# Optimization experiments

Hardware: AMD Instinct MI355X
Metric: run time of the kernel (lower is better)

## Reference

```python
import jax, jax.numpy as jnp
import numpy as np

CUTN = 32
CUT_SIZE = 224
CUT_POW = 1.0


def _adaptive_avg_pool2d(crop, out_size):
    """Faithful torch F.adaptive_avg_pool2d for a square NCHW crop (static size).
    Uses a summed-area table so each output pixel averages the exact torch bin
    [floor(i*S/out), ceil((i+1)*S/out))."""
    S = crop.shape[2]
    idx = np.arange(out_size)
    s = (idx * S) // out_size                       # bin starts
    e = ((idx + 1) * S + out_size - 1) // out_size  # bin ends (ceil)
    # summed-area table, padded so P[..., i, j] = sum over crop[..., :i, :j]
    P = jnp.pad(jnp.cumsum(jnp.cumsum(crop, axis=2), axis=3),
                ((0, 0), (0, 0), (1, 0), (1, 0)))
    A = (P[:, :, e][:, :, :, e] - P[:, :, s][:, :, :, e]
         - P[:, :, e][:, :, :, s] + P[:, :, s][:, :, :, s])
    cnt = (e - s).astype(np.float32)
    return A / jnp.asarray(np.outer(cnt, cnt), crop.dtype)


def setup_inputs() -> dict:
    key = jax.random.key(0)
    B, C, H, W = 8, 3, 512, 512
    x = jax.random.normal(key, (B, C, H, W), dtype=jnp.float32)
    # Replicate torch's host-side RNG with a fixed numpy generator so sizes and
    # offsets are deterministic constants (in-range by construction).
    rng = np.random.default_rng(0)
    max_size = min(H, W)
    min_size = min(H, W, CUT_SIZE)
    sizes, oy, ox = [], [], []
    for _ in range(CUTN):
        sz = int(rng.random() ** CUT_POW * (max_size - min_size) + min_size)
        sizes.append(sz)
        oy.append(int(rng.integers(0, H - sz + 1)))
        ox.append(int(rng.integers(0, W - sz + 1)))
    return {
        "x": x,
        "sizes": jnp.asarray(sizes, jnp.int32),
        "offsets_y": jnp.asarray(oy, jnp.int32),
        "offsets_x": jnp.asarray(ox, jnp.int32),
        "cut_size": CUT_SIZE,
    }


def reference(x, sizes, offsets_y, offsets_x, cut_size):
    B, C, _, _ = x.shape
    sizes_np = np.asarray(sizes)
    oy_np = np.asarray(offsets_y)
    ox_np = np.asarray(offsets_x)
    cutouts = []
    for i in range(sizes_np.shape[0]):  # loop over fixed cutn (structural)
        sz = int(sizes_np[i])
        crop = jax.lax.dynamic_slice(
            x, (0, 0, int(oy_np[i]), int(ox_np[i])), (B, C, sz, sz))
        cutouts.append(_adaptive_avg_pool2d(crop, cut_size))
    return jnp.concatenate(cutouts, axis=0)  # [cutn*B, C, cut_size, cut_size]
```

## Files before the change

### kernel.cpp

```cpp
#include <hip/hip_runtime.h>


typedef float f32x4 __attribute__((ext_vector_type(4)));

constexpr int OUTSZ = 224;
constexpr int BB    = 8;
constexpr int CC    = 3;
constexpr int HH    = 512;
constexpr int WW    = 512;
constexpr int CUTN  = 32;

constexpr int TP     = 8;
constexpr int NBAND  = OUTSZ / TP;
constexpr int LDSF   = TP * WW + 8;
constexpr int NPLANE = BB * CC;
constexpr int WPP    = CUTN * NBAND;
constexpr int NBLOCKS = NPLANE * WPP;
constexpr int NXCD   = 8;
constexpr int CHUNK  = NBLOCKS / NXCD;

template <int WIN>
__device__ __forceinline__ void pool_cols(const float* __restrict__ tile,
                                          float* __restrict__ outp,
                                          int base, const float* __restrict__ w)
{
#pragma unroll
    for (int k = 0; k < TP; ++k) {
        const float* tr = tile + k * WW + base;
        float s = tr[0] * w[0];
        s = fmaf(tr[1], w[1], s);
        s = fmaf(tr[2], w[2], s);
        if (WIN == 4) s = fmaf(tr[3], w[3], s);
        outp[(size_t)k * OUTSZ] = s;
    }
}

__global__ __launch_bounds__(256, 8) void make_cutouts_kernel(
    const float* __restrict__ x,
    const int*   __restrict__ sizes,
    const int*   __restrict__ offy,
    const int*   __restrict__ offx,
    float*       __restrict__ out)
{
    __shared__ float tile[LDSF];

    int gid = blockIdx.x;
    int w   = (gid % NXCD) * CHUNK + gid / NXCD;

    int plane = w / WPP;
    int rest  = w - plane * WPP;
    int i     = rest / NBAND;
    int tb    = rest - i * NBAND;
    int b     = plane / CC;
    int c     = plane - b * CC;

    int S  = sizes[i];
    int y0 = offy[i];
    int x0 = offx[i];
    int p0 = tb * TP;
    int tid = threadIdx.x;

    const float* plane_p = x + (size_t)(plane * HH + y0) * WW;

    if (tid < 8) tile[TP * WW + tid] = 0.0f;

    int wv   = __builtin_amdgcn_readfirstlane(tid >> 6);
    int lane = tid & 63;
    int vo   = ((wv & 1) << 6) + lane;
    f32x4* tile4 = (f32x4*)tile;
#pragma unroll
    for (int j = 0; j < 4; ++j) {
        int k  = (wv >> 1) + 2 * j;
        int p  = p0 + k;
        int rs = (p * S) / OUTSZ;
        int wp = ((p + 1) * S + OUTSZ - 1) / OUTSZ - rs;
        const f32x4* rp = (const f32x4*)(plane_p + (size_t)rs * WW);
        f32x4 a = rp[vo];
        f32x4 v1, v2, v3;
        bool b1 = wp > 1, b2 = wp > 2, b3 = wp > 3;
        if (b1) v1 = rp[vo + 128];
        if (b2) v2 = rp[vo + 256];
        if (b3) v3 = rp[vo + 384];
        if (b1) a += v1;
        if (b2) a += v2;
        if (b3) a += v3;
        float iv = (wp == 1) ? 1.0f : (wp == 2) ? 0.5f
                 : (wp == 3) ? (1.0f / 3.0f) : 0.25f;
        a *= iv;
        tile4[k * 128 + vo] = a;
    }
    __syncthreads();

    if (tid < OUTSZ) {
        int q  = tid;
        int sq = (q * S) / OUTSZ;
        int wq = ((q + 1) * S + OUTSZ - 1) / OUTSZ - sq;
        float invq = (wq == 1) ? 1.0f : (wq == 2) ? 0.5f
                   : (wq == 3) ? (1.0f / 3.0f) : 0.25f;
        float wt[4];
        wt[0] = invq;
        wt[1] = (wq > 1) ? invq : 0.0f;
        wt[2] = (wq > 2) ? invq : 0.0f;
        wt[3] = (wq > 3) ? invq : 0.0f;
        float* outp = out
            + ((size_t)((i * BB + b) * CC + c) * OUTSZ + p0) * OUTSZ + q;
        if (S <= 2 * OUTSZ)
            pool_cols<3>(tile, outp, x0 + sq, wt);
        else
            pool_cols<4>(tile, outp, x0 + sq, wt);
    }
}

extern "C" void kernel_launch(void* const* d_in, const int* in_sizes, int n_in,
                              void* d_out, int out_size, void* d_ws, size_t ws_size,
                              hipStream_t stream) {
    const float* x     = (const float*)d_in[0];
    const int*   sizes = (const int*)d_in[1];
    const int*   offy  = (const int*)d_in[2];
    const int*   offx  = (const int*)d_in[3];
    float* out = (float*)d_out;

    make_cutouts_kernel<<<NBLOCKS, 256, 0, stream>>>(x, sizes, offy, offx, out);
}
```

Before: 194.0 us.

## Make each block loop over all bands with double-buffered LDS pipeline

Switches from one block per 8-row band to one block per (plane, cutout) that walks all 28 bands. Global loads for band k+2 are issued into registers while band k+1 is written to LDS and band k is pooled, using a double-buffered tile. This hides global load latency within a block and amortizes setup such as the column weights. In exchange there are only 768 blocks, with more LDS and registers per block and lower occupancy (launch bounds 3), so less parallelism is available to hide latency.

```diff
diff --git a/kernel.cpp b/kernel.cpp
--- a/kernel.cpp
+++ b/kernel.cpp
@@ -12,21 +12,60 @@
 
 constexpr int TP     = 8;
 constexpr int NBAND  = OUTSZ / TP;
-constexpr int LDSF   = TP * WW + 8;
+constexpr int TILEF  = TP * WW + 8;
 constexpr int NPLANE = BB * CC;
-constexpr int WPP    = CUTN * NBAND;
-constexpr int NBLOCKS = NPLANE * WPP;
+constexpr int NBLOCKS = NPLANE * CUTN;
 constexpr int NXCD   = 8;
 constexpr int CHUNK  = NBLOCKS / NXCD;
 
+__device__ __forceinline__ void stage_issue(const float* __restrict__ plane_p,
+                                            int S, int p0, int wv, int vo,
+                                            f32x4 (&v)[4][4])
+{
+#pragma unroll
+    for (int j = 0; j < 4; ++j) {
+        int k  = (wv >> 1) + 2 * j;
+        int p  = p0 + k;
+        int rs = (p * S) / OUTSZ;
+        int wp = ((p + 1) * S + OUTSZ - 1) / OUTSZ - rs;
+        const f32x4* rp = (const f32x4*)(plane_p + (size_t)rs * WW);
+        v[j][0] = rp[vo];
+        if (wp > 1) v[j][1] = rp[vo + 128];
+        if (wp > 2) v[j][2] = rp[vo + 256];
+        if (wp > 3) v[j][3] = rp[vo + 384];
+    }
+}
+
+__device__ __forceinline__ void stage_write(float* __restrict__ buf,
+                                            int S, int p0, int wv, int vo,
+                                            f32x4 (&v)[4][4])
+{
+    f32x4* t4 = (f32x4*)buf;
+#pragma unroll
+    for (int j = 0; j < 4; ++j) {
+        int k  = (wv >> 1) + 2 * j;
+        int p  = p0 + k;
+        int rs = (p * S) / OUTSZ;
+        int wp = ((p + 1) * S + OUTSZ - 1) / OUTSZ - rs;
+        f32x4 a = v[j][0];
+        if (wp > 1) a += v[j][1];
+        if (wp > 2) a += v[j][2];
+        if (wp > 3) a += v[j][3];
+        float iv = (wp == 1) ? 1.0f : (wp == 2) ? 0.5f
+                 : (wp == 3) ? (1.0f / 3.0f) : 0.25f;
+        a *= iv;
+        t4[k * 128 + vo] = a;
+    }
+}
+
 template <int WIN>
-__device__ __forceinline__ void pool_cols(const float* __restrict__ tile,
+__device__ __forceinline__ void pool_band(const float* __restrict__ buf,
                                           float* __restrict__ outp,
                                           int base, const float* __restrict__ w)
 {
 #pragma unroll
     for (int k = 0; k < TP; ++k) {
-        const float* tr = tile + k * WW + base;
+        const float* tr = buf + k * WW + base;
         float s = tr[0] * w[0];
         s = fmaf(tr[1], w[1], s);
         s = fmaf(tr[2], w[2], s);
@@ -35,80 +74,85 @@
     }
 }
 
-__global__ __launch_bounds__(256, 8) void make_cutouts_kernel(
+__device__ __forceinline__ void band_barrier()
+{
+    asm volatile("s_waitcnt lgkmcnt(0)" ::: "memory");
+    __builtin_amdgcn_s_barrier();
+}
+
+template <int WIN>
+__device__ __forceinline__ void run_bands(const float* __restrict__ plane_p,
+                                          float (*tile)[TILEF],
+                                          float* __restrict__ outp,
+                                          int S, int wv, int vo, int tid,
+                                          int base, const float* __restrict__ wt,
+                                          f32x4 (&v)[4][4])
+{
+    for (int k = 0; k < NBAND; ++k) {
+        if (k + 1 < NBAND)
+            stage_write(tile[(k + 1) & 1], S, (k + 1) * TP, wv, vo, v);
+        if (k + 2 < NBAND)
+            stage_issue(plane_p, S, (k + 2) * TP, wv, vo, v);
+        if (tid < OUTSZ)
+            pool_band<WIN>(tile[k & 1], outp + (size_t)k * TP * OUTSZ, base, wt);
+        band_barrier();
+    }
+}
+
+__global__ __launch_bounds__(256, 3) void make_cutouts_kernel(
     const float* __restrict__ x,
     const int*   __restrict__ sizes,
     const int*   __restrict__ offy,
     const int*   __restrict__ offx,
     float*       __restrict__ out)
 {
-    __shared__ float tile[LDSF];
+    __shared__ float tile[2][TILEF];
 
     int gid = blockIdx.x;
     int w   = (gid % NXCD) * CHUNK + gid / NXCD;
-
-    int plane = w / WPP;
-    int rest  = w - plane * WPP;
-    int i     = rest / NBAND;
-    int tb    = rest - i * NBAND;
+    int plane = w / CUTN;
+    int i     = w - plane * CUTN;
     int b     = plane / CC;
     int c     = plane - b * CC;
 
     int S  = sizes[i];
     int y0 = offy[i];
     int x0 = offx[i];
-    int p0 = tb * TP;
     int tid = threadIdx.x;
 
     const float* plane_p = x + (size_t)(plane * HH + y0) * WW;
 
-    if (tid < 8) tile[TP * WW + tid] = 0.0f;
+    if (tid < 8) {
+        tile[0][TP * WW + tid] = 0.0f;
+        tile[1][TP * WW + tid] = 0.0f;
+    }
 
     int wv   = __builtin_amdgcn_readfirstlane(tid >> 6);
     int lane = tid & 63;
     int vo   = ((wv & 1) << 6) + lane;
-    f32x4* tile4 = (f32x4*)tile;
-#pragma unroll
-    for (int j = 0; j < 4; ++j) {
-        int k  = (wv >> 1) + 2 * j;
-        int p  = p0 + k;
-        int rs = (p * S) / OUTSZ;
-        int wp = ((p + 1) * S + OUTSZ - 1) / OUTSZ - rs;
-        const f32x4* rp = (const f32x4*)(plane_p + (size_t)rs * WW);
-        f32x4 a = rp[vo];
-        f32x4 v1, v2, v3;
-        bool b1 = wp > 1, b2 = wp > 2, b3 = wp > 3;
-        if (b1) v1 = rp[vo + 128];
-        if (b2) v2 = rp[vo + 256];
-        if (b3) v3 = rp[vo + 384];
-        if (b1) a += v1;
-        if (b2) a += v2;
-        if (b3) a += v3;
-        float iv = (wp == 1) ? 1.0f : (wp == 2) ? 0.5f
-                 : (wp == 3) ? (1.0f / 3.0f) : 0.25f;
-        a *= iv;
-        tile4[k * 128 + vo] = a;
-    }
-    __syncthreads();
 
-    if (tid < OUTSZ) {
-        int q  = tid;
-        int sq = (q * S) / OUTSZ;
-        int wq = ((q + 1) * S + OUTSZ - 1) / OUTSZ - sq;
-        float invq = (wq == 1) ? 1.0f : (wq == 2) ? 0.5f
-                   : (wq == 3) ? (1.0f / 3.0f) : 0.25f;
-        float wt[4];
-        wt[0] = invq;
-        wt[1] = (wq > 1) ? invq : 0.0f;
-        wt[2] = (wq > 2) ? invq : 0.0f;
-        wt[3] = (wq > 3) ? invq : 0.0f;
-        float* outp = out
-            + ((size_t)((i * BB + b) * CC + c) * OUTSZ + p0) * OUTSZ + q;
-        if (S <= 2 * OUTSZ)
-            pool_cols<3>(tile, outp, x0 + sq, wt);
-        else
-            pool_cols<4>(tile, outp, x0 + sq, wt);
-    }
+    int sq = (tid * S) / OUTSZ;
+    int wq = ((tid + 1) * S + OUTSZ - 1) / OUTSZ - sq;
+    float invq = (wq == 1) ? 1.0f : (wq == 2) ? 0.5f
+               : (wq == 3) ? (1.0f / 3.0f) : 0.25f;
+    float wt[4];
+    wt[0] = invq;
+    wt[1] = (wq > 1) ? invq : 0.0f;
+    wt[2] = (wq > 2) ? invq : 0.0f;
+    wt[3] = (wq > 3) ? invq : 0.0f;
+    int base = x0 + sq;
+    float* outp = out + ((size_t)((i * BB + b) * CC + c) * OUTSZ) * OUTSZ + tid;
+
+    f32x4 v[4][4];
+    stage_issue(plane_p, S, 0, wv, vo, v);
+    stage_write(tile[0], S, 0, wv, vo, v);
+    stage_issue(plane_p, S, TP, wv, vo, v);
+    band_barrier();
+
+    if (S <= 2 * OUTSZ)
+        run_bands<3>(plane_p, tile, outp, S, wv, vo, tid, base, wt, v);
+    else
+        run_bands<4>(plane_p, tile, outp, S, wv, vo, tid, base, wt, v);
 }
 
 extern "C" void kernel_launch(void* const* d_in, const int* in_sizes, int n_in,
```

Result: slower. 220.3 us (+13.5%).

## Make each wavefront process its own output rows with double-buffered LDS slices

Applied to the files above, without the earlier changes.

Each wavefront now independently processes 4 output rows, using its own double-buffered LDS row slice instead of a shared 8-row tile. This removes the block-wide __syncthreads. It also prefetches the next row's global loads into registers while the current row is pooled along x. Block size per band grows to 16 rows, so there are half as many blocks. The per-wave scheme depends on wave-synchronous LDS visibility without a barrier, and it uses more registers.

```diff
diff --git a/kernel.cpp b/kernel.cpp
--- a/kernel.cpp
+++ b/kernel.cpp
@@ -10,28 +10,88 @@
 constexpr int WW    = 512;
 constexpr int CUTN  = 32;
 
-constexpr int TP     = 8;
-constexpr int NBAND  = OUTSZ / TP;
-constexpr int LDSF   = TP * WW + 8;
+constexpr int RPB    = 16;
+constexpr int RPW    = 4;
+constexpr int NCH    = OUTSZ / RPB;
+constexpr int SLICEF = WW + 8;
 constexpr int NPLANE = BB * CC;
-constexpr int WPP    = CUTN * NBAND;
-constexpr int NBLOCKS = NPLANE * WPP;
+constexpr int NBLOCKS = NPLANE * CUTN * NCH;
 constexpr int NXCD   = 8;
-constexpr int CHUNK  = NBLOCKS / NXCD;
+constexpr int CHUNKSZ = NBLOCKS / NXCD;
+
+__device__ __forceinline__ void load_row(const float* __restrict__ plane_p,
+                                         int S, int p, int lane, f32x4 (&v)[8])
+{
+    int rs = (p * S) / OUTSZ;
+    int wp = ((p + 1) * S + OUTSZ - 1) / OUTSZ - rs;
+    const f32x4* rp = (const f32x4*)(plane_p + (size_t)rs * WW);
+    int c0 = lane;
+    int c1 = lane + 64;
+    v[0] = rp[c0];        v[1] = rp[c1];
+    if (wp > 1) { v[2] = rp[c0 + 128]; v[3] = rp[c1 + 128]; }
+    if (wp > 2) { v[4] = rp[c0 + 256]; v[5] = rp[c1 + 256]; }
+    if (wp > 3) { v[6] = rp[c0 + 384]; v[7] = rp[c1 + 384]; }
+}
+
+__device__ __forceinline__ void reduce_write(float* __restrict__ buf,
+                                             int S, int p, int lane,
+                                             f32x4 (&v)[8])
+{
+    int rs = (p * S) / OUTSZ;
+    int wp = ((p + 1) * S + OUTSZ - 1) / OUTSZ - rs;
+    f32x4 a0 = v[0], a1 = v[1];
+    if (wp > 1) { a0 += v[2]; a1 += v[3]; }
+    if (wp > 2) { a0 += v[4]; a1 += v[5]; }
+    if (wp > 3) { a0 += v[6]; a1 += v[7]; }
+    float iv = (wp == 1) ? 1.0f : (wp == 2) ? 0.5f
+             : (wp == 3) ? (1.0f / 3.0f) : 0.25f;
+    a0 *= iv; a1 *= iv;
+    f32x4* t4 = (f32x4*)buf;
+    t4[lane] = a0;
+    t4[lane + 64] = a1;
+}
 
 template <int WIN>
-__device__ __forceinline__ void pool_cols(const float* __restrict__ tile,
-                                          float* __restrict__ outp,
-                                          int base, const float* __restrict__ w)
+__device__ __forceinline__ void pool_row(const float* __restrict__ buf,
+                                         float* __restrict__ outrow,
+                                         int x0, int lane,
+                                         const int* __restrict__ sqv,
+                                         const int* __restrict__ wqv,
+                                         const float* __restrict__ invqv)
 {
 #pragma unroll
-    for (int k = 0; k < TP; ++k) {
-        const float* tr = tile + k * WW + base;
-        float s = tr[0] * w[0];
-        s = fmaf(tr[1], w[1], s);
-        s = fmaf(tr[2], w[2], s);
-        if (WIN == 4) s = fmaf(tr[3], w[3], s);
-        outp[(size_t)k * OUTSZ] = s;
+    for (int m = 0; m < 4; ++m) {
+        if (m == 3 && lane >= 32) break;
+        const float* tr = buf + x0 + sqv[m];
+        float z = 0.0f;
+        float s = tr[0];
+        s += (wqv[m] > 1) ? tr[1] : z;
+        s += (wqv[m] > 2) ? tr[2] : z;
+        if (WIN == 4) s += (wqv[m] > 3) ? tr[3] : z;
+        outrow[lane + 64 * m] = s * invqv[m];
+    }
+}
+
+template <int WIN>
+__device__ __forceinline__ void run_rows(const float* __restrict__ plane_p,
+                                         float* __restrict__ s0,
+                                         float* __restrict__ s1,
+                                         float* __restrict__ outbase,
+                                         int S, int x0, int p0, int lane,
+                                         const int* __restrict__ sqv,
+                                         const int* __restrict__ wqv,
+                                         const float* __restrict__ invqv)
+{
+    f32x4 v[8];
+    load_row(plane_p, S, p0, lane, v);
+#pragma unroll
+    for (int r = 0; r < RPW; ++r) {
+        float* buf = (r & 1) ? s1 : s0;
+        reduce_write(buf, S, p0 + r, lane, v);
+        if (r + 1 < RPW)
+            load_row(plane_p, S, p0 + r + 1, lane, v);
+        pool_row<WIN>(buf, outbase + (size_t)(p0 + r) * OUTSZ,
+                      x0, lane, sqv, wqv, invqv);
     }
 }
 
@@ -42,73 +102,50 @@
     const int*   __restrict__ offx,
     float*       __restrict__ out)
 {
-    __shared__ float tile[LDSF];
+    __shared__ float lds[4][2][SLICEF];
 
     int gid = blockIdx.x;
-    int w   = (gid % NXCD) * CHUNK + gid / NXCD;
-
-    int plane = w / WPP;
-    int rest  = w - plane * WPP;
-    int i     = rest / NBAND;
-    int tb    = rest - i * NBAND;
+    int w   = (gid % NXCD) * CHUNKSZ + gid / NXCD;
+    int plane = w / (CUTN * NCH);
+    int rest  = w - plane * (CUTN * NCH);
+    int i     = rest / NCH;
+    int ch    = rest - i * NCH;
     int b     = plane / CC;
     int c     = plane - b * CC;
 
     int S  = sizes[i];
     int y0 = offy[i];
     int x0 = offx[i];
-    int p0 = tb * TP;
-    int tid = threadIdx.x;
+    int tid  = threadIdx.x;
+    int wv   = __builtin_amdgcn_readfirstlane(tid >> 6);
+    int lane = tid & 63;
+    int p0   = ch * RPB + wv * RPW;
 
     const float* plane_p = x + (size_t)(plane * HH + y0) * WW;
+    float* s0 = &lds[wv][0][0];
+    float* s1 = &lds[wv][1][0];
 
-    if (tid < 8) tile[TP * WW + tid] = 0.0f;
+    int   sqv[4];
+    int   wqv[4];
+    float invqv[4];
+#pragma unroll
+    for (int m = 0; m < 4; ++m) {
+        int q = lane + 64 * m;
+        int qq = (q < OUTSZ) ? q : 0;
+        int sq = (qq * S) / OUTSZ;
+        int wq = ((qq + 1) * S + OUTSZ - 1) / OUTSZ - sq;
+        sqv[m] = sq;
+        wqv[m] = wq;
+        invqv[m] = (wq == 1) ? 1.0f : (wq == 2) ? 0.5f
+                 : (wq == 3) ? (1.0f / 3.0f) : 0.25f;
+    }
 
-    int wv   = __builtin_amdgcn_readfirstlane(tid >> 6);
-    int lane = tid & 63;
-    int vo   = ((wv & 1) << 6) + lane;
-    f32x4* tile4 = (f32x4*)tile;
-#pragma unroll
-    for (int j = 0; j < 4; ++j) {
-        int k  = (wv >> 1) + 2 * j;
-        int p  = p0 + k;
-        int rs = (p * S) / OUTSZ;
-        int wp = ((p + 1) * S + OUTSZ - 1) / OUTSZ - rs;
-        const f32x4* rp = (const f32x4*)(plane_p + (size_t)rs * WW);
-        f32x4 a = rp[vo];
-        f32x4 v1, v2, v3;
-        bool b1 = wp > 1, b2 = wp > 2, b3 = wp > 3;
-        if (b1) v1 = rp[vo + 128];
-        if (b2) v2 = rp[vo + 256];
-        if (b3) v3 = rp[vo + 384];
-        if (b1) a += v1;
-        if (b2) a += v2;
-        if (b3) a += v3;
-        float iv = (wp == 1) ? 1.0f : (wp == 2) ? 0.5f
-                 : (wp == 3) ? (1.0f / 3.0f) : 0.25f;
-        a *= iv;
-        tile4[k * 128 + vo] = a;
-    }
-    __syncthreads();
+    float* outbase = out + (size_t)((i * BB + b) * CC + c) * OUTSZ * OUTSZ;
 
-    if (tid < OUTSZ) {
-        int q  = tid;
-        int sq = (q * S) / OUTSZ;
-        int wq = ((q + 1) * S + OUTSZ - 1) / OUTSZ - sq;
-        float invq = (wq == 1) ? 1.0f : (wq == 2) ? 0.5f
-                   : (wq == 3) ? (1.0f / 3.0f) : 0.25f;
-        float wt[4];
-        wt[0] = invq;
-        wt[1] = (wq > 1) ? invq : 0.0f;
-        wt[2] = (wq > 2) ? invq : 0.0f;
-        wt[3] = (wq > 3) ? invq : 0.0f;
-        float* outp = out
-            + ((size_t)((i * BB + b) * CC + c) * OUTSZ + p0) * OUTSZ + q;
-        if (S <= 2 * OUTSZ)
-            pool_cols<3>(tile, outp, x0 + sq, wt);
-        else
-            pool_cols<4>(tile, outp, x0 + sq, wt);
-    }
+    if (S <= 2 * OUTSZ)
+        run_rows<3>(plane_p, s0, s1, outbase, S, x0, p0, lane, sqv, wqv, invqv);
+    else
+        run_rows<4>(plane_p, s0, s1, outbase, S, x0, p0, lane, sqv, wqv, invqv);
 }
 
 extern "C" void kernel_launch(void* const* d_in, const int* in_sizes, int n_in,
```

Result: slower. 247.5 us (+27.5%).

## Split row band into two halves and overlap second-half loads with first-half pooling

Applied to the files above, without the earlier changes.

The 8-row band is processed in two halves of 4 rows. The global loads for the second half are issued into registers before the first half is written to LDS and column-pooled, so memory latency is hidden behind the first half's pooling and stores. A custom barrier waits only on LDS counters rather than doing a full syncthreads. This raises register pressure (two sets of 8 f32x4 load buffers) under the 8-blocks-per-SM launch bound, and adds a second barrier per block.

```diff
diff --git a/kernel.cpp b/kernel.cpp
--- a/kernel.cpp
+++ b/kernel.cpp
@@ -19,20 +19,87 @@
 constexpr int NXCD   = 8;
 constexpr int CHUNK  = NBLOCKS / NXCD;
 
-template <int WIN>
-__device__ __forceinline__ void pool_cols(const float* __restrict__ tile,
-                                          float* __restrict__ outp,
-                                          int base, const float* __restrict__ w)
+__device__ __forceinline__ void half_issue(const float* __restrict__ plane_p,
+                                           int S, int p0h, int wv, int vo,
+                                           f32x4 (&v)[2][4])
 {
 #pragma unroll
-    for (int k = 0; k < TP; ++k) {
-        const float* tr = tile + k * WW + base;
+    for (int j = 0; j < 2; ++j) {
+        int k  = (wv >> 1) + 2 * j;
+        int p  = p0h + k;
+        int rs = (p * S) / OUTSZ;
+        int wp = ((p + 1) * S + OUTSZ - 1) / OUTSZ - rs;
+        const f32x4* rp = (const f32x4*)(plane_p + (size_t)rs * WW);
+        v[j][0] = rp[vo];
+        if (wp > 1) v[j][1] = rp[vo + 128];
+        if (wp > 2) v[j][2] = rp[vo + 256];
+        if (wp > 3) v[j][3] = rp[vo + 384];
+    }
+}
+
+__device__ __forceinline__ void half_write(float* __restrict__ tile,
+                                           int S, int p0h, int rowoff,
+                                           int wv, int vo, f32x4 (&v)[2][4])
+{
+    f32x4* t4 = (f32x4*)tile;
+#pragma unroll
+    for (int j = 0; j < 2; ++j) {
+        int k  = (wv >> 1) + 2 * j;
+        int p  = p0h + k;
+        int rs = (p * S) / OUTSZ;
+        int wp = ((p + 1) * S + OUTSZ - 1) / OUTSZ - rs;
+        f32x4 a = v[j][0];
+        if (wp > 1) a += v[j][1];
+        if (wp > 2) a += v[j][2];
+        if (wp > 3) a += v[j][3];
+        float iv = (wp == 1) ? 1.0f : (wp == 2) ? 0.5f
+                 : (wp == 3) ? (1.0f / 3.0f) : 0.25f;
+        a *= iv;
+        t4[(rowoff + k) * 128 + vo] = a;
+    }
+}
+
+template <int WIN>
+__device__ __forceinline__ void pool_half(const float* __restrict__ tile,
+                                          float* __restrict__ outp,
+                                          int rowoff, int base,
+                                          const float* __restrict__ w)
+{
+#pragma unroll
+    for (int k = 0; k < 4; ++k) {
+        const float* tr = tile + (rowoff + k) * WW + base;
         float s = tr[0] * w[0];
         s = fmaf(tr[1], w[1], s);
         s = fmaf(tr[2], w[2], s);
         if (WIN == 4) s = fmaf(tr[3], w[3], s);
         outp[(size_t)k * OUTSZ] = s;
     }
+}
+
+__device__ __forceinline__ void lgkm_barrier()
+{
+    asm volatile("s_waitcnt lgkmcnt(0)" ::: "memory");
+    __builtin_amdgcn_s_barrier();
+}
+
+template <int WIN>
+__device__ __forceinline__ void run_block(const float* __restrict__ plane_p,
+                                          float* __restrict__ tile,
+                                          float* __restrict__ outp,
+                                          int S, int p0, int wv, int vo,
+                                          int tid, int base,
+                                          const float* __restrict__ wt,
+                                          f32x4 (&vA)[2][4], f32x4 (&vB)[2][4])
+{
+    half_write(tile, S, p0, 0, wv, vo, vA);
+    half_issue(plane_p, S, p0 + 4, wv, vo, vB);
+    lgkm_barrier();
+    if (tid < OUTSZ)
+        pool_half<WIN>(tile, outp, 0, base, wt);
+    half_write(tile, S, p0 + 4, 4, wv, vo, vB);
+    lgkm_barrier();
+    if (tid < OUTSZ)
+        pool_half<WIN>(tile, outp + (size_t)4 * OUTSZ, 4, base, wt);
 }
 
 __global__ __launch_bounds__(256, 8) void make_cutouts_kernel(
@@ -46,7 +113,6 @@
 
     int gid = blockIdx.x;
     int w   = (gid % NXCD) * CHUNK + gid / NXCD;
-
     int plane = w / WPP;
     int rest  = w - plane * WPP;
     int i     = rest / NBAND;
@@ -62,53 +128,32 @@
 
     const float* plane_p = x + (size_t)(plane * HH + y0) * WW;
 
-    if (tid < 8) tile[TP * WW + tid] = 0.0f;
-
     int wv   = __builtin_amdgcn_readfirstlane(tid >> 6);
     int lane = tid & 63;
     int vo   = ((wv & 1) << 6) + lane;
-    f32x4* tile4 = (f32x4*)tile;
-#pragma unroll
-    for (int j = 0; j < 4; ++j) {
-        int k  = (wv >> 1) + 2 * j;
-        int p  = p0 + k;
-        int rs = (p * S) / OUTSZ;
-        int wp = ((p + 1) * S + OUTSZ - 1) / OUTSZ - rs;
-        const f32x4* rp = (const f32x4*)(plane_p + (size_t)rs * WW);
-        f32x4 a = rp[vo];
-        f32x4 v1, v2, v3;
-        bool b1 = wp > 1, b2 = wp > 2, b3 = wp > 3;
-        if (b1) v1 = rp[vo + 128];
-        if (b2) v2 = rp[vo + 256];
-        if (b3) v3 = rp[vo + 384];
-        if (b1) a += v1;
-        if (b2) a += v2;
-        if (b3) a += v3;
-        float iv = (wp == 1) ? 1.0f : (wp == 2) ? 0.5f
-                 : (wp == 3) ? (1.0f / 3.0f) : 0.25f;
-        a *= iv;
-        tile4[k * 128 + vo] = a;
-    }
-    __syncthreads();
 
-    if (tid < OUTSZ) {
-        int q  = tid;
-        int sq = (q * S) / OUTSZ;
-        int wq = ((q + 1) * S + OUTSZ - 1) / OUTSZ - sq;
-        float invq = (wq == 1) ? 1.0f : (wq == 2) ? 0.5f
-                   : (wq == 3) ? (1.0f / 3.0f) : 0.25f;
-        float wt[4];
-        wt[0] = invq;
-        wt[1] = (wq > 1) ? invq : 0.0f;
-        wt[2] = (wq > 2) ? invq : 0.0f;
-        wt[3] = (wq > 3) ? invq : 0.0f;
-        float* outp = out
-            + ((size_t)((i * BB + b) * CC + c) * OUTSZ + p0) * OUTSZ + q;
-        if (S <= 2 * OUTSZ)
-            pool_cols<3>(tile, outp, x0 + sq, wt);
-        else
-            pool_cols<4>(tile, outp, x0 + sq, wt);
-    }
+    f32x4 vA[2][4], vB[2][4];
+    half_issue(plane_p, S, p0, wv, vo, vA);
+
+    if (tid < 8) tile[TP * WW + tid] = 0.0f;
+
+    int sq = (tid * S) / OUTSZ;
+    int wq = ((tid + 1) * S + OUTSZ - 1) / OUTSZ - sq;
+    float invq = (wq == 1) ? 1.0f : (wq == 2) ? 0.5f
+               : (wq == 3) ? (1.0f / 3.0f) : 0.25f;
+    float wt[4];
+    wt[0] = invq;
+    wt[1] = (wq > 1) ? invq : 0.0f;
+    wt[2] = (wq > 2) ? invq : 0.0f;
+    wt[3] = (wq > 3) ? invq : 0.0f;
+    int base = x0 + sq;
+    float* outp = out
+        + ((size_t)((i * BB + b) * CC + c) * OUTSZ + p0) * OUTSZ + tid;
+
+    if (S <= 2 * OUTSZ)
+        run_block<3>(plane_p, tile, outp, S, p0, wv, vo, tid, base, wt, vA, vB);
+    else
+        run_block<4>(plane_p, tile, outp, S, p0, wv, vo, tid, base, wt, vA, vB);
 }
 
 extern "C" void kernel_launch(void* const* d_in, const int* in_sizes, int n_in,
```

After: 204.0 us. 1.05x slower.
